# Performance work log

Hardware: AMD Instinct MI355X
Metric: run time of the kernel (lower is better)

The kernel has to match this reference:

```python
import jax, jax.numpy as jnp
import numpy as np

IGNORE_INDEX = 255
LOG_CLAMP = 100.0  # torch BCE clamps log at -100, so -log(x) <= 100


def _neg_log(x, cond):
    # BCE(x, 1) = -log(x), with the torch clamp log(x) >= -100.
    x_safe = jnp.where(cond, jnp.maximum(x, 1e-38), 1.0)
    return jnp.where(cond, jnp.minimum(-jnp.log(x_safe), LOG_CLAMP), 0.0)


def setup_inputs() -> dict:
    key = jax.random.key(0)
    k1, k2 = jax.random.split(key)
    B, C, H, W, D = 1, 20, 256, 256, 32
    pred = jax.random.normal(k1, (B, C, H, W, D), dtype=jnp.float32)
    target = jax.random.randint(k2, (B, H, W, D), 0, C, dtype=jnp.int64)
    return {"pred": pred, "target": target}


def reference(pred, target):
    C = pred.shape[1]
    p = jax.nn.softmax(pred, axis=1)                      # [B,C,H,W,D]
    mask = (target != IGNORE_INDEX)                        # [B,H,W,D]

    # Flatten voxels: [N, C] probs, [N] labels, [N] mask.
    p_flat = jnp.moveaxis(p, 1, -1).reshape(-1, C)
    t_flat = target.reshape(-1)
    m_flat = mask.reshape(-1).astype(p.dtype)
    t_safe = jnp.where(mask.reshape(-1), t_flat, 0).astype(jnp.int32)

    # Per-class reductions in one pass (replaces the per-class python loop):
    # nominator[c] = sum_{masked, t==c} p_c ; ct_count[c] = |{masked, t==c}|
    p_at_t = jnp.take_along_axis(p_flat, t_safe[:, None], axis=1)[:, 0] * m_flat
    nominator = jax.ops.segment_sum(p_at_t, t_safe, num_segments=C)
    ct_count = jax.ops.segment_sum(m_flat, t_safe, num_segments=C)
    sum_p = jnp.einsum('nc,n->c', p_flat, m_flat)          # sum of p_c over masked
    n_masked = jnp.sum(m_flat)

    neg_count = n_masked - ct_count                        # sum(1 - ct)
    spec_num = n_masked - sum_p - ct_count + nominator     # sum((1-p)(1-ct))

    valid = ct_count > 0
    prec = nominator / jnp.maximum(sum_p, 1e-38)
    rec = nominator / jnp.maximum(ct_count, 1.0)
    spec = spec_num / jnp.maximum(neg_count, 1.0)

    loss_c = (_neg_log(prec, valid & (sum_p > 0))
              + _neg_log(rec, valid)
              + _neg_log(spec, valid & (neg_count > 0)))
    count = jnp.sum(valid.astype(p.dtype))
    return jnp.sum(loss_c) / count
```

## Files before the change

### kernel.cpp

```cpp
#include <hip/hip_runtime.h>
#include <math.h>

#define NCLS 20
#define IGNORE_IDX 255
#define LOG2E 1.4426950408889634f

__device__ __forceinline__ float wave_reduce(float v) {
#pragma unroll
  for (int off = 32; off > 0; off >>= 1) v += __shfl_xor(v, off, 64);
  return v;
}

__device__ __forceinline__ float neg_log_clamped(float x, bool cond) {
  if (!cond) return 0.0f;
  float xs = fmaxf(x, 1e-38f);
  return fminf(-logf(xs), 100.0f);
}

__global__ __launch_bounds__(256) void pass1(const float* __restrict__ pred,
                                             const int* __restrict__ target,
                                             float* __restrict__ ws, int N) {
  __shared__ float s_acc[3 * NCLS];
  const int tid = threadIdx.x;
  for (int i = tid; i < 3 * NCLS; i += blockDim.x) s_acc[i] = 0.0f;
  __syncthreads();

  float acc[NCLS];
#pragma unroll
  for (int c = 0; c < NCLS; ++c) acc[c] = 0.0f;

  const int nq = N >> 2;
  const int stride = gridDim.x * blockDim.x;
  for (int q = blockIdx.x * blockDim.x + tid; q < nq; q += stride) {
    const int n = q << 2;
    float4 x[NCLS];
#pragma unroll
    for (int c = 0; c < NCLS; ++c)
      x[c] = *reinterpret_cast<const float4*>(pred + (size_t)c * N + n);

    float4 m = x[0];
#pragma unroll
    for (int c = 1; c < NCLS; ++c) {
      m.x = fmaxf(m.x, x[c].x);
      m.y = fmaxf(m.y, x[c].y);
      m.z = fmaxf(m.z, x[c].z);
      m.w = fmaxf(m.w, x[c].w);
    }

    const int4 t4 = *reinterpret_cast<const int4*>(target + n);

    float4 s = make_float4(0.0f, 0.0f, 0.0f, 0.0f);
    float pt0 = 0.0f, pt1 = 0.0f, pt2 = 0.0f, pt3 = 0.0f;
#pragma unroll
    for (int c = 0; c < NCLS; ++c) {
      x[c].x = __builtin_amdgcn_exp2f((x[c].x - m.x) * LOG2E);
      x[c].y = __builtin_amdgcn_exp2f((x[c].y - m.y) * LOG2E);
      x[c].z = __builtin_amdgcn_exp2f((x[c].z - m.z) * LOG2E);
      x[c].w = __builtin_amdgcn_exp2f((x[c].w - m.w) * LOG2E);
      s.x += x[c].x; s.y += x[c].y; s.z += x[c].z; s.w += x[c].w;
      pt0 = (c == t4.x) ? x[c].x : pt0;
      pt1 = (c == t4.y) ? x[c].y : pt1;
      pt2 = (c == t4.z) ? x[c].z : pt2;
      pt3 = (c == t4.w) ? x[c].w : pt3;
    }

    const float r0 = __builtin_amdgcn_rcpf(s.x);
    const float r1 = __builtin_amdgcn_rcpf(s.y);
    const float r2 = __builtin_amdgcn_rcpf(s.z);
    const float r3 = __builtin_amdgcn_rcpf(s.w);

    const bool m0 = (t4.x != IGNORE_IDX);
    const bool m1 = (t4.y != IGNORE_IDX);
    const bool m2 = (t4.z != IGNORE_IDX);
    const bool m3 = (t4.w != IGNORE_IDX);
    const float w0 = m0 ? r0 : 0.0f;
    const float w1 = m1 ? r1 : 0.0f;
    const float w2 = m2 ? r2 : 0.0f;
    const float w3 = m3 ? r3 : 0.0f;

#pragma unroll
    for (int c = 0; c < NCLS; ++c)
      acc[c] += x[c].x * w0 + x[c].y * w1 + x[c].z * w2 + x[c].w * w3;

    if (m0) { atomicAdd(&s_acc[NCLS + t4.x], pt0 * w0); atomicAdd(&s_acc[2 * NCLS + t4.x], 1.0f); }
    if (m1) { atomicAdd(&s_acc[NCLS + t4.y], pt1 * w1); atomicAdd(&s_acc[2 * NCLS + t4.y], 1.0f); }
    if (m2) { atomicAdd(&s_acc[NCLS + t4.z], pt2 * w2); atomicAdd(&s_acc[2 * NCLS + t4.z], 1.0f); }
    if (m3) { atomicAdd(&s_acc[NCLS + t4.w], pt3 * w3); atomicAdd(&s_acc[2 * NCLS + t4.w], 1.0f); }
  }

#pragma unroll
  for (int c = 0; c < NCLS; ++c) {
    float v = wave_reduce(acc[c]);
    if ((tid & 63) == 0) atomicAdd(&s_acc[c], v);
  }
  __syncthreads();

  if (tid < 3 * NCLS) atomicAdd(&ws[tid], s_acc[tid]);
}

__global__ __launch_bounds__(64) void pass2(const float* __restrict__ ws,
                                            float* __restrict__ out) {
  const int lane = threadIdx.x;
  const float cnt = (lane < NCLS) ? ws[2 * NCLS + lane] : 0.0f;
  const float n_masked = wave_reduce(cnt);

  float loss = 0.0f, validf = 0.0f;
  if (lane < NCLS) {
    const float sump = ws[lane];
    const float nom = ws[NCLS + lane];
    const bool valid = cnt > 0.0f;
    const float prec = nom / fmaxf(sump, 1e-38f);
    const float rec = nom / fmaxf(cnt, 1.0f);
    const float negc = n_masked - cnt;
    const float specn = n_masked - sump - cnt + nom;
    const float spec = specn / fmaxf(negc, 1.0f);
    loss = neg_log_clamped(prec, valid && (sump > 0.0f)) +
           neg_log_clamped(rec, valid) +
           neg_log_clamped(spec, valid && (negc > 0.0f));
    validf = valid ? 1.0f : 0.0f;
  }
  loss = wave_reduce(loss);
  validf = wave_reduce(validf);
  if (lane == 0) out[0] = loss / validf;
}

extern "C" void kernel_launch(void* const* d_in, const int* in_sizes, int n_in,
                              void* d_out, int out_size, void* d_ws, size_t ws_size,
                              hipStream_t stream) {
  const float* pred = (const float*)d_in[0];
  const int* target = (const int*)d_in[1];
  const int N = in_sizes[1];
  float* ws = (float*)d_ws;

  hipMemsetAsync(d_ws, 0, 3 * NCLS * sizeof(float), stream);
  pass1<<<768, 256, 0, stream>>>(pred, target, ws, N);
  pass2<<<1, 64, 0, stream>>>(ws, (float*)d_out);
}
```

Before: 254.2 us.

## Fuse reduction and finalize into one kernel with last-block pattern and nontemporal loads

Merges the memset, the partial-reduction kernel and the finalize kernel into a single launch. Each block writes its partials to a per-block slot, and the last block to arrive, detected with a global atomic counter, reduces all slots and computes the loss. Prediction loads become nontemporal, and the grid shrinks from 768 to 512 blocks. This removes two launches and the global float atomics, at the cost of a serial tail reduction in one block and fewer blocks in flight.

```diff
diff --git a/kernel.cpp b/kernel.cpp
--- a/kernel.cpp
+++ b/kernel.cpp
@@ -4,6 +4,13 @@
 #define NCLS 20
 #define IGNORE_IDX 255
 #define LOG2E 1.4426950408889634f
+#define NBLK 512
+#define NTHR 256
+
+typedef float v4f __attribute__((ext_vector_type(4)));
+typedef int v4i __attribute__((ext_vector_type(4)));
+
+__device__ int g_cnt;
 
 __device__ __forceinline__ float wave_reduce(float v) {
 #pragma unroll
@@ -17,12 +24,16 @@
   return fminf(-logf(xs), 100.0f);
 }
 
-__global__ __launch_bounds__(256) void pass1(const float* __restrict__ pred,
-                                             const int* __restrict__ target,
-                                             float* __restrict__ ws, int N) {
+__global__ __launch_bounds__(NTHR) void fused(const float* __restrict__ pred,
+                                              const int* __restrict__ target,
+                                              float* __restrict__ ws,
+                                              float* __restrict__ out, int N) {
   __shared__ float s_acc[3 * NCLS];
+  __shared__ float s_fin[64];
+  __shared__ int s_last;
   const int tid = threadIdx.x;
-  for (int i = tid; i < 3 * NCLS; i += blockDim.x) s_acc[i] = 0.0f;
+  for (int i = tid; i < 3 * NCLS; i += NTHR) s_acc[i] = 0.0f;
+  if (tid < 64) s_fin[tid] = 0.0f;
   __syncthreads();
 
   float acc[NCLS];
@@ -30,62 +41,56 @@
   for (int c = 0; c < NCLS; ++c) acc[c] = 0.0f;
 
   const int nq = N >> 2;
-  const int stride = gridDim.x * blockDim.x;
-  for (int q = blockIdx.x * blockDim.x + tid; q < nq; q += stride) {
+  const int tot = NBLK * NTHR;
+  for (int q = blockIdx.x * NTHR + tid; q < nq; q += tot) {
     const int n = q << 2;
-    float4 x[NCLS];
+    v4f x[NCLS];
 #pragma unroll
     for (int c = 0; c < NCLS; ++c)
-      x[c] = *reinterpret_cast<const float4*>(pred + (size_t)c * N + n);
+      x[c] = __builtin_nontemporal_load(
+          reinterpret_cast<const v4f*>(pred + (size_t)c * N + n));
 
-    float4 m = x[0];
+    v4f m = x[0];
 #pragma unroll
     for (int c = 1; c < NCLS; ++c) {
-      m.x = fmaxf(m.x, x[c].x);
-      m.y = fmaxf(m.y, x[c].y);
-      m.z = fmaxf(m.z, x[c].z);
-      m.w = fmaxf(m.w, x[c].w);
+#pragma unroll
+      for (int j = 0; j < 4; ++j) m[j] = fmaxf(m[j], x[c][j]);
     }
 
-    const int4 t4 = *reinterpret_cast<const int4*>(target + n);
+    const v4i t4 = *reinterpret_cast<const v4i*>(target + n);
 
-    float4 s = make_float4(0.0f, 0.0f, 0.0f, 0.0f);
-    float pt0 = 0.0f, pt1 = 0.0f, pt2 = 0.0f, pt3 = 0.0f;
+    v4f s = (v4f)(0.0f);
+    v4f pt = (v4f)(0.0f);
 #pragma unroll
     for (int c = 0; c < NCLS; ++c) {
-      x[c].x = __builtin_amdgcn_exp2f((x[c].x - m.x) * LOG2E);
-      x[c].y = __builtin_amdgcn_exp2f((x[c].y - m.y) * LOG2E);
-      x[c].z = __builtin_amdgcn_exp2f((x[c].z - m.z) * LOG2E);
-      x[c].w = __builtin_amdgcn_exp2f((x[c].w - m.w) * LOG2E);
-      s.x += x[c].x; s.y += x[c].y; s.z += x[c].z; s.w += x[c].w;
-      pt0 = (c == t4.x) ? x[c].x : pt0;
-      pt1 = (c == t4.y) ? x[c].y : pt1;
-      pt2 = (c == t4.z) ? x[c].z : pt2;
-      pt3 = (c == t4.w) ? x[c].w : pt3;
+#pragma unroll
+      for (int j = 0; j < 4; ++j) {
+        x[c][j] = __builtin_amdgcn_exp2f((x[c][j] - m[j]) * LOG2E);
+        s[j] += x[c][j];
+        pt[j] = (c == t4[j]) ? x[c][j] : pt[j];
+      }
     }
 
-    const float r0 = __builtin_amdgcn_rcpf(s.x);
-    const float r1 = __builtin_amdgcn_rcpf(s.y);
-    const float r2 = __builtin_amdgcn_rcpf(s.z);
-    const float r3 = __builtin_amdgcn_rcpf(s.w);
-
-    const bool m0 = (t4.x != IGNORE_IDX);
-    const bool m1 = (t4.y != IGNORE_IDX);
-    const bool m2 = (t4.z != IGNORE_IDX);
-    const bool m3 = (t4.w != IGNORE_IDX);
-    const float w0 = m0 ? r0 : 0.0f;
-    const float w1 = m1 ? r1 : 0.0f;
-    const float w2 = m2 ? r2 : 0.0f;
-    const float w3 = m3 ? r3 : 0.0f;
+    float w[4];
+    bool msk[4];
+#pragma unroll
+    for (int j = 0; j < 4; ++j) {
+      msk[j] = (t4[j] != IGNORE_IDX);
+      const float r = __builtin_amdgcn_rcpf(s[j]);
+      w[j] = msk[j] ? r : 0.0f;
+    }
 
 #pragma unroll
     for (int c = 0; c < NCLS; ++c)
-      acc[c] += x[c].x * w0 + x[c].y * w1 + x[c].z * w2 + x[c].w * w3;
+      acc[c] += x[c][0] * w[0] + x[c][1] * w[1] + x[c][2] * w[2] + x[c][3] * w[3];
 
-    if (m0) { atomicAdd(&s_acc[NCLS + t4.x], pt0 * w0); atomicAdd(&s_acc[2 * NCLS + t4.x], 1.0f); }
-    if (m1) { atomicAdd(&s_acc[NCLS + t4.y], pt1 * w1); atomicAdd(&s_acc[2 * NCLS + t4.y], 1.0f); }
-    if (m2) { atomicAdd(&s_acc[NCLS + t4.z], pt2 * w2); atomicAdd(&s_acc[2 * NCLS + t4.z], 1.0f); }
-    if (m3) { atomicAdd(&s_acc[NCLS + t4.w], pt3 * w3); atomicAdd(&s_acc[2 * NCLS + t4.w], 1.0f); }
+#pragma unroll
+    for (int j = 0; j < 4; ++j) {
+      if (msk[j]) {
+        atomicAdd(&s_acc[NCLS + t4[j]], pt[j] * w[j]);
+        atomicAdd(&s_acc[2 * NCLS + t4[j]], 1.0f);
+      }
+    }
   }
 
 #pragma unroll
@@ -95,33 +100,51 @@
   }
   __syncthreads();
 
-  if (tid < 3 * NCLS) atomicAdd(&ws[tid], s_acc[tid]);
-}
+  if (tid < 64)
+    ws[(size_t)blockIdx.x * 64 + tid] = (tid < 3 * NCLS) ? s_acc[tid] : 0.0f;
+  __threadfence();
+  __syncthreads();
 
-__global__ __launch_bounds__(64) void pass2(const float* __restrict__ ws,
-                                            float* __restrict__ out) {
-  const int lane = threadIdx.x;
-  const float cnt = (lane < NCLS) ? ws[2 * NCLS + lane] : 0.0f;
-  const float n_masked = wave_reduce(cnt);
+  if (tid == 0) {
+    int old = __hip_atomic_fetch_add(&g_cnt, 1, __ATOMIC_ACQ_REL,
+                                     __HIP_MEMORY_SCOPE_AGENT);
+    s_last = (old == (int)gridDim.x - 1);
+    if (s_last)
+      __hip_atomic_store(&g_cnt, 0, __ATOMIC_RELAXED, __HIP_MEMORY_SCOPE_AGENT);
+  }
+  __syncthreads();
+  if (!s_last) return;
 
-  float loss = 0.0f, validf = 0.0f;
-  if (lane < NCLS) {
-    const float sump = ws[lane];
-    const float nom = ws[NCLS + lane];
-    const bool valid = cnt > 0.0f;
-    const float prec = nom / fmaxf(sump, 1e-38f);
-    const float rec = nom / fmaxf(cnt, 1.0f);
-    const float negc = n_masked - cnt;
-    const float specn = n_masked - sump - cnt + nom;
-    const float spec = specn / fmaxf(negc, 1.0f);
-    loss = neg_log_clamped(prec, valid && (sump > 0.0f)) +
-           neg_log_clamped(rec, valid) +
-           neg_log_clamped(spec, valid && (negc > 0.0f));
-    validf = valid ? 1.0f : 0.0f;
+  __threadfence();
+
+  float a = 0.0f;
+  const int total = NBLK * 64;
+  for (int i = tid; i < total; i += NTHR) a += ws[i];
+  atomicAdd(&s_fin[tid & 63], a);
+  __syncthreads();
+
+  if (tid < 64) {
+    const float cnt = (tid < NCLS) ? s_fin[2 * NCLS + tid] : 0.0f;
+    const float n_masked = wave_reduce(cnt);
+    float loss = 0.0f, validf = 0.0f;
+    if (tid < NCLS) {
+      const float sump = s_fin[tid];
+      const float nom = s_fin[NCLS + tid];
+      const bool valid = cnt > 0.0f;
+      const float prec = nom / fmaxf(sump, 1e-38f);
+      const float rec = nom / fmaxf(cnt, 1.0f);
+      const float negc = n_masked - cnt;
+      const float specn = n_masked - sump - cnt + nom;
+      const float spec = specn / fmaxf(negc, 1.0f);
+      loss = neg_log_clamped(prec, valid && (sump > 0.0f)) +
+             neg_log_clamped(rec, valid) +
+             neg_log_clamped(spec, valid && (negc > 0.0f));
+      validf = valid ? 1.0f : 0.0f;
+    }
+    loss = wave_reduce(loss);
+    validf = wave_reduce(validf);
+    if (tid == 0) out[0] = loss / validf;
   }
-  loss = wave_reduce(loss);
-  validf = wave_reduce(validf);
-  if (lane == 0) out[0] = loss / validf;
 }
 
 extern "C" void kernel_launch(void* const* d_in, const int* in_sizes, int n_in,
@@ -130,9 +153,5 @@
   const float* pred = (const float*)d_in[0];
   const int* target = (const int*)d_in[1];
   const int N = in_sizes[1];
-  float* ws = (float*)d_ws;
-
-  hipMemsetAsync(d_ws, 0, 3 * NCLS * sizeof(float), stream);
-  pass1<<<768, 256, 0, stream>>>(pred, target, ws, N);
-  pass2<<<1, 64, 0, stream>>>(ws, (float*)d_out);
+  fused<<<NBLK, NTHR, 0, stream>>>(pred, target, (float*)d_ws, (float*)d_out, N);
 }
```

Result: slower. 296.9 us (+16.8%).
